# Optimization experiments

Hardware: AMD Instinct MI355X
Metric: run time of the kernel (lower is better)

Reference implementation:

```python
import jax, jax.numpy as jnp
import numpy as np

C = 64
D = C // 8  # query/key channels
B, H, W = 4, 64, 64


def setup_inputs() -> dict:
    key = jax.random.key(0)
    ks = jax.random.split(key, 8)
    x = jax.random.normal(ks[0], (B, C, H, W), dtype=jnp.float32)
    # 1x1 conv params (kernel squeezed to [out_ch, in_ch])
    sq = 1.0 / np.sqrt(C)
    Wq = jax.random.uniform(ks[1], (D, C), jnp.float32, -sq, sq)
    bq = jax.random.uniform(ks[2], (D,), jnp.float32, -sq, sq)
    Wk = jax.random.uniform(ks[3], (D, C), jnp.float32, -sq, sq)
    bk = jax.random.uniform(ks[4], (D,), jnp.float32, -sq, sq)
    Wv = jax.random.uniform(ks[5], (C, C), jnp.float32, -sq, sq)
    bv = jax.random.uniform(ks[6], (C,), jnp.float32, -sq, sq)
    # gamma is zero-initialized in the module; use a nonzero value so the
    # attention path actually contributes to the output.
    gamma = jax.random.normal(ks[7], (1,), dtype=jnp.float32)
    return {"x": x, "Wq": Wq, "bq": bq, "Wk": Wk, "bk": bk, "Wv": Wv, "bv": bv, "gamma": gamma}


def reference(x, Wq, bq, Wk, bk, Wv, bv, gamma):
    b, c, h, w = x.shape
    n = h * w
    xf = x.reshape(b, c, n)                                   # [B,C,N]
    q = jnp.einsum('dc,bcn->bdn', Wq, xf) + bq[None, :, None]  # [B,D,N]
    k = jnp.einsum('dc,bcn->bdn', Wk, xf) + bk[None, :, None]  # [B,D,N]
    v = jnp.einsum('ec,bcn->ben', Wv, xf) + bv[None, :, None]  # [B,C,N]
    energy = jnp.einsum('bdn,bdm->bnm', q, k)                  # [B,N,N] = Q^T K
    attn = jax.nn.softmax(energy, axis=-1)                     # softmax over keys m
    # out[b,c,n] = sum_m v[b,c,m] * attn[b,n,m]  (V @ attention^T in torch)
    out = jnp.einsum('bcm,bnm->bcn', v, attn).reshape(b, c, h, w)
    return gamma[0] * out + x
```

## Files before the change

### kernel.cpp

```cpp
#include <hip/hip_runtime.h>
#include <hip/hip_bf16.h>
#include <math.h>

#define BB 4
#define CC 64
#define DD 8
#define NN 4096
#define KS 8
#define KPS (NN / KS)
#define VSTR 260
#define KSTR 12
#define LOG2E 1.44269504088896340736f

typedef __attribute__((ext_vector_type(4))) short short4v;
typedef __attribute__((ext_vector_type(4))) unsigned short ushort4v;
typedef __attribute__((ext_vector_type(8))) unsigned short ushort8;
typedef __attribute__((ext_vector_type(16))) float f32x16;

#if defined(__HIP_DEVICE_COMPILE__)
  #if __has_builtin(__builtin_amdgcn_mfma_f32_32x32x8bf16_1k)
    #define MFMA32x8(A, B, C) __builtin_amdgcn_mfma_f32_32x32x8bf16_1k(A, B, C, 0, 0, 0)
  #elif __has_builtin(__builtin_amdgcn_mfma_f32_32x32x8_bf16)
    #define MFMA32x8(A, B, C) __builtin_amdgcn_mfma_f32_32x32x8_bf16(A, B, C, 0, 0, 0)
  #else
    #error "no 32x32x8 bf16 MFMA builtin in device pass"
  #endif
  #if __has_builtin(__builtin_amdgcn_exp2f)
    #define EXP2(x) __builtin_amdgcn_exp2f(x)
  #else
    #define EXP2(x) exp2f(x)
  #endif
#else
  static __device__ __host__ inline f32x16 MFMA32x8(short4v, short4v, f32x16 c) { return c; }
  #define EXP2(x) exp2f(x)
#endif

static __device__ inline short4v pack4(float a, float b, float c, float d) {
    union { short4v s; __hip_bfloat162 h[2]; } u;
    u.h[0] = __float22bfloat162_rn(make_float2(a, b));
    u.h[1] = __float22bfloat162_rn(make_float2(c, d));
    return u.s;
}
static __device__ inline unsigned packu(float lo, float hi) {
    union { __hip_bfloat162 h; unsigned u; } t;
    t.h = __float22bfloat162_rn(make_float2(lo, hi));
    return t.u;
}

__global__ __launch_bounds__(256) void qkv_kernel(
    const float* __restrict__ x,  const float* __restrict__ Wq, const float* __restrict__ bq,
    const float* __restrict__ Wk, const float* __restrict__ bk,
    const float* __restrict__ Wv, const float* __restrict__ bv,
    unsigned short* __restrict__ qb, unsigned short* __restrict__ kb,
    unsigned short* __restrict__ vT)
{
    __shared__ unsigned short LQ[128 * 8];
    __shared__ unsigned short LK[128 * 8];

    int tid = threadIdx.x;
    int wave = tid >> 6, lane = tid & 63;
    int l32 = lane & 31, h2 = lane >> 5;

    int blk = blockIdx.x;
    int b = blk & (BB - 1);
    int r2 = blk >> 2;
    int rt = r2 % 3;
    int ng = r2 / 3;
    int n0 = ng * 128 + wave * 32;

    short4v af[8];
    #pragma unroll
    for (int s = 0; s < 8; ++s) {
        float4 w4;
        if (rt < 2) {
            w4 = *(const float4*)(Wv + (size_t)(rt * 32 + l32) * CC + s * 8 + 4 * h2);
        } else if (l32 < 8) {
            w4 = *(const float4*)(Wq + (size_t)l32 * CC + s * 8 + 4 * h2);
        } else if (l32 < 16) {
            w4 = *(const float4*)(Wk + (size_t)(l32 - 8) * CC + s * 8 + 4 * h2);
        } else {
            w4 = make_float4(0.f, 0.f, 0.f, 0.f);
        }
        af[s] = pack4(w4.x, w4.y, w4.z, w4.w);
    }

    const float* xb = x + (size_t)b * CC * NN + n0 + l32;
    short4v bf[8];
    #pragma unroll
    for (int s = 0; s < 8; ++s) {
        int c0 = s * 8 + 4 * h2;
        float x0 = xb[(size_t)(c0 + 0) * NN];
        float x1 = xb[(size_t)(c0 + 1) * NN];
        float x2 = xb[(size_t)(c0 + 2) * NN];
        float x3 = xb[(size_t)(c0 + 3) * NN];
        bf[s] = pack4(x0, x1, x2, x3);
    }

    f32x16 acc;
    #pragma unroll
    for (int r = 0; r < 16; ++r) acc[r] = 0.f;
    #pragma unroll
    for (int s = 0; s < 8; ++s)
        acc = MFMA32x8(af[s], bf[s], acc);

    if (rt < 2) {
        #pragma unroll
        for (int r = 0; r < 16; ++r) {
            int row = rt * 32 + (r & 3) + 8 * (r >> 2) + 4 * h2;
            float val = acc[r] + bv[row];
            __hip_bfloat16 hv = __float2bfloat16(val);
            vT[((size_t)b * CC + row) * NN + n0 + l32] = *(unsigned short*)&hv;
        }
    } else {
        short4v qp = pack4((acc[0] + bq[0 + 4 * h2]) * LOG2E,
                           (acc[1] + bq[1 + 4 * h2]) * LOG2E,
                           (acc[2] + bq[2 + 4 * h2]) * LOG2E,
                           (acc[3] + bq[3 + 4 * h2]) * LOG2E);
        short4v kp = pack4(acc[4] + bk[0 + 4 * h2],
                           acc[5] + bk[1 + 4 * h2],
                           acc[6] + bk[2 + 4 * h2],
                           acc[7] + bk[3 + 4 * h2]);
        int nl = wave * 32 + l32;
        *(short4v*)(LQ + (size_t)nl * 8 + 4 * h2) = qp;
        *(short4v*)(LK + (size_t)nl * 8 + 4 * h2) = kp;
        __syncthreads();
        if (tid < 128) {
            ushort8 row = *(const ushort8*)(LQ + (size_t)tid * 8);
            *(ushort8*)(qb + ((size_t)b * NN + ng * 128 + tid) * 8) = row;
        } else {
            int t = tid - 128;
            ushort8 row = *(const ushort8*)(LK + (size_t)t * 8);
            *(ushort8*)(kb + ((size_t)b * NN + ng * 128 + t) * 8) = row;
        }
    }
}

__global__ __launch_bounds__(256, 4) void flash_kernel(
    const unsigned short* __restrict__ qb, const unsigned short* __restrict__ kb,
    const unsigned short* __restrict__ vT, unsigned* __restrict__ accb,
    float* __restrict__ sbuf)
{
    __shared__ unsigned short VS[64 * VSTR];
    __shared__ unsigned short KL[256 * KSTR];
    int tid = threadIdx.x;
    int wave = tid >> 6, lane = tid & 63;
    int l32 = lane & 31, h2 = lane >> 5;

    int blk = blockIdx.x;
    int b = blk & (BB - 1);
    int rest = blk >> 2;
    int split = rest & (KS - 1);
    int qchunk = rest >> 3;
    int n0 = qchunk * 128 + wave * 32;

    short4v qf = *(const short4v*)(qb + ((size_t)b * NN + n0 + l32) * DD + h2 * 4);

    const unsigned short* kbb = kb + (size_t)b * NN * DD;
    const unsigned short* vbb = vT + (size_t)b * CC * NN;
    int m0 = split * KPS;

    int chb = wave * 16 + h2;

    f32x16 o0, o1, zz;
    #pragma unroll
    for (int r = 0; r < 16; ++r) { o0[r] = 0.f; o1[r] = 0.f; zz[r] = 0.f; }
    float s0 = 0.f, s1 = 0.f, s2 = 0.f, s3 = 0.f;

    ushort8 vA[8];
    #pragma unroll
    for (int i = 0; i < 8; ++i)
        vA[i] = *(const ushort8*)(vbb + (size_t)(chb + 2 * i) * NN + m0 + l32 * 8);
    ushort8 kA = *(const ushort8*)(kbb + (size_t)(m0 + tid) * DD);
    #pragma unroll
    for (int i = 0; i < 8; ++i) {
        unsigned short* p = VS + (size_t)(chb + 2 * i) * VSTR + l32 * 8;
        *(ushort4v*)(p)     = *(ushort4v*)&vA[i];
        *(ushort4v*)(p + 4) = *((ushort4v*)&vA[i] + 1);
    }
    {
        unsigned short* p = KL + (size_t)tid * KSTR;
        *(ushort4v*)(p)     = *(ushort4v*)&kA;
        *(ushort4v*)(p + 4) = *((ushort4v*)&kA + 1);
    }
    __syncthreads();

    int mB = m0 + 256;
    ushort8 vB[8];
    #pragma unroll
    for (int i = 0; i < 8; ++i)
        vB[i] = *(const ushort8*)(vbb + (size_t)(chb + 2 * i) * NN + mB + l32 * 8);
    ushort8 kB = *(const ushort8*)(kbb + (size_t)(mB + tid) * DD);

    #pragma unroll
    for (int ph = 0; ph < 2; ++ph) {
        #pragma unroll
        for (int s = 0; s < 8; ++s) {
            short4v kf = *(const short4v*)(KL + (size_t)(s * 32 + l32) * KSTR + h2 * 4);
            f32x16 st = MFMA32x8(kf, qf, zz);
            float w[16];
            #pragma unroll
            for (int r = 0; r < 16; ++r) w[r] = EXP2(st[r]);
            s0 += (w[0] + w[1]) + (w[2] + w[3]);
            s1 += (w[4] + w[5]) + (w[6] + w[7]);
            s2 += (w[8] + w[9]) + (w[10] + w[11]);
            s3 += (w[12] + w[13]) + (w[14] + w[15]);

            union { short4v s; __hip_bfloat162 h[2]; } u[4];
            #pragma unroll
            for (int g = 0; g < 4; ++g) {
                u[g].h[0] = __float22bfloat162_rn(make_float2(w[4 * g],     w[4 * g + 1]));
                u[g].h[1] = __float22bfloat162_rn(make_float2(w[4 * g + 2], w[4 * g + 3]));
            }
            #pragma unroll
            for (int g = 0; g < 4; ++g) {
                int gg = s * 4 + g;
                short4v vf0 = *(const short4v*)(VS + (size_t)(l32)      * VSTR + gg * 8 + h2 * 4);
                short4v vf1 = *(const short4v*)(VS + (size_t)(32 + l32) * VSTR + gg * 8 + h2 * 4);
                o0 = MFMA32x8(u[g].s, vf0, o0);
                o1 = MFMA32x8(u[g].s, vf1, o1);
            }
        }
        if (ph == 0) {
            __syncthreads();
            #pragma unroll
            for (int i = 0; i < 8; ++i) {
                unsigned short* p = VS + (size_t)(chb + 2 * i) * VSTR + l32 * 8;
                *(ushort4v*)(p)     = *(ushort4v*)&vB[i];
                *(ushort4v*)(p + 4) = *((ushort4v*)&vB[i] + 1);
            }
            unsigned short* p = KL + (size_t)tid * KSTR;
            *(ushort4v*)(p)     = *(ushort4v*)&kB;
            *(ushort4v*)(p + 4) = *((ushort4v*)&kB + 1);
            __syncthreads();
        }
    }

    unsigned* au = accb + (((size_t)((b * KS + split) * 128 + qchunk * 4 + wave)) << 10);
    #pragma unroll
    for (int r = 0; r < 16; ++r)
        au[r * 64 + lane] = packu(o0[r], o1[r]);

    float ssum = (s0 + s1) + (s2 + s3);
    ssum += __shfl_xor(ssum, 32);
    if (lane < 32)
        sbuf[(size_t)(b * KS + split) * NN + n0 + l32] = ssum;
}

__global__ __launch_bounds__(256) void norm_kernel(
    const unsigned* __restrict__ accb, const float* __restrict__ sbuf,
    const float* __restrict__ x, const float* __restrict__ gamma,
    float* __restrict__ out)
{
    __shared__ float tile[32 * 65];
    __shared__ float stl[32];
    int blk = blockIdx.x;
    int b = blk >> 7;
    int g = blk & 127;
    int n0 = g * 32;
    int tid = threadIdx.x;

    if (tid < 32) {
        float st = 0.f;
        #pragma unroll
        for (int sp = 0; sp < KS; ++sp)
            st += sbuf[(size_t)(b * KS + sp) * NN + n0 + tid];
        stl[tid] = 1.0f / st;
    }

    int r = tid >> 4;
    int lane0 = (tid & 15) * 4;
    int h2 = lane0 >> 5;
    int qi = (r & 3) + 8 * (r >> 2) + 4 * h2;

    float alo[4], ahi[4];
    #pragma unroll
    for (int e = 0; e < 4; ++e) { alo[e] = 0.f; ahi[e] = 0.f; }
    #pragma unroll
    for (int sp = 0; sp < KS; ++sp) {
        const unsigned* base = accb + (((size_t)((b * KS + sp) * 128 + g)) << 10);
        uint4 v = *(const uint4*)(base + tid * 4);
        unsigned ws[4] = {v.x, v.y, v.z, v.w};
        #pragma unroll
        for (int e = 0; e < 4; ++e) {
            alo[e] += __uint_as_float(ws[e] << 16);
            ahi[e] += __uint_as_float(ws[e] & 0xFFFF0000u);
        }
    }
    #pragma unroll
    for (int e = 0; e < 4; ++e) {
        int cl = (lane0 + e) & 31;
        tile[qi * 65 + cl]      = alo[e];
        tile[qi * 65 + 32 + cl] = ahi[e];
    }
    __syncthreads();

    float gm = gamma[0];
    #pragma unroll
    for (int p = 0; p < 8; ++p) {
        int idx = p * 256 + tid;
        int c = idx >> 5, n_l = idx & 31;
        size_t xi = ((size_t)b * CC + c) * NN + n0 + n_l;
        out[xi] = gm * tile[n_l * 65 + c] * stl[n_l] + x[xi];
    }
}

extern "C" void kernel_launch(void* const* d_in, const int* in_sizes, int n_in,
                              void* d_out, int out_size, void* d_ws, size_t ws_size,
                              hipStream_t stream)
{
    const float* x     = (const float*)d_in[0];
    const float* Wq    = (const float*)d_in[1];
    const float* bq    = (const float*)d_in[2];
    const float* Wk    = (const float*)d_in[3];
    const float* bk    = (const float*)d_in[4];
    const float* Wv    = (const float*)d_in[5];
    const float* bv    = (const float*)d_in[6];
    const float* gamma = (const float*)d_in[7];
    float* out = (float*)d_out;

    float* ws = (float*)d_ws;
    size_t off = 0;
    unsigned short* qb = (unsigned short*)(ws + off); off += (size_t)BB * NN * DD / 2 + 64;
    unsigned short* kb = (unsigned short*)(ws + off); off += (size_t)BB * NN * DD / 2 + 64;
    unsigned short* vT = (unsigned short*)(ws + off); off += (size_t)BB * CC * NN / 2 + 64;
    unsigned* accb = (unsigned*)(ws + off); off += (size_t)BB * KS * NN * CC / 2;
    float* sbuf = ws + off; off += (size_t)BB * KS * NN;

    qkv_kernel<<<BB * 3 * 32, 256, 0, stream>>>(x, Wq, bq, Wk, bk, Wv, bv, qb, kb, vT);
    flash_kernel<<<BB * (NN / 128) * KS, 256, 0, stream>>>(qb, kb, vT, accb, sbuf);
    norm_kernel<<<BB * 128, 256, 0, stream>>>(accb, sbuf, x, gamma, out);
}
```

Measured before the change: 113.4 us.

## Use 512-thread flash blocks with 16 key splits and single-tile staging

Doubles the key-split count to 16 so each block processes one 256-key tile, and doubles the block to 512 threads (8 waves, 256 queries) so each staged K/V tile in LDS is reused by twice as many query rows. The two-phase double-buffered load is replaced by one cooperative load followed by the compute loop. This reduces K/V global reads per query and removes the mid-kernel barrier pair. In exchange it doubles the partial-accumulator and row-sum traffic the norm kernel must reduce, and it no longer overlaps loads with compute.

```diff
diff --git a/kernel.cpp b/kernel.cpp
--- a/kernel.cpp
+++ b/kernel.cpp
@@ -6,7 +6,7 @@
 #define CC 64
 #define DD 8
 #define NN 4096
-#define KS 8
+#define KS 16
 #define KPS (NN / KS)
 #define VSTR 260
 #define KSTR 12
@@ -135,7 +135,7 @@
     }
 }
 
-__global__ __launch_bounds__(256, 4) void flash_kernel(
+__global__ __launch_bounds__(512, 8) void flash_kernel(
     const unsigned short* __restrict__ qb, const unsigned short* __restrict__ kb,
     const unsigned short* __restrict__ vT, unsigned* __restrict__ accb,
     float* __restrict__ sbuf)
@@ -150,8 +150,8 @@
     int b = blk & (BB - 1);
     int rest = blk >> 2;
     int split = rest & (KS - 1);
-    int qchunk = rest >> 3;
-    int n0 = qchunk * 128 + wave * 32;
+    int qchunk = rest >> 4;
+    int n0 = qchunk * 256 + wave * 32;
 
     short4v qf = *(const short4v*)(qb + ((size_t)b * NN + n0 + l32) * DD + h2 * 4);
 
@@ -159,83 +159,67 @@
     const unsigned short* vbb = vT + (size_t)b * CC * NN;
     int m0 = split * KPS;
 
-    int chb = wave * 16 + h2;
+    int ch = tid >> 3, ks0 = (tid & 7) * 32;
+    {
+        const unsigned short* vg = vbb + (size_t)ch * NN + m0 + ks0;
+        ushort8 v0 = *(const ushort8*)(vg);
+        ushort8 v1 = *(const ushort8*)(vg + 8);
+        ushort8 v2 = *(const ushort8*)(vg + 16);
+        ushort8 v3 = *(const ushort8*)(vg + 24);
+        ushort8 kA = {0,0,0,0,0,0,0,0};
+        if (tid < 256) kA = *(const ushort8*)(kbb + (size_t)(m0 + tid) * DD);
+
+        unsigned short* vp = VS + (size_t)ch * VSTR + ks0;
+        *(ushort4v*)(vp)      = *(ushort4v*)&v0;
+        *(ushort4v*)(vp + 4)  = *((ushort4v*)&v0 + 1);
+        *(ushort4v*)(vp + 8)  = *(ushort4v*)&v1;
+        *(ushort4v*)(vp + 12) = *((ushort4v*)&v1 + 1);
+        *(ushort4v*)(vp + 16) = *(ushort4v*)&v2;
+        *(ushort4v*)(vp + 20) = *((ushort4v*)&v2 + 1);
+        *(ushort4v*)(vp + 24) = *(ushort4v*)&v3;
+        *(ushort4v*)(vp + 28) = *((ushort4v*)&v3 + 1);
+        if (tid < 256) {
+            unsigned short* p = KL + (size_t)tid * KSTR;
+            *(ushort4v*)(p)     = *(ushort4v*)&kA;
+            *(ushort4v*)(p + 4) = *((ushort4v*)&kA + 1);
+        }
+    }
+    __syncthreads();
 
     f32x16 o0, o1, zz;
     #pragma unroll
     for (int r = 0; r < 16; ++r) { o0[r] = 0.f; o1[r] = 0.f; zz[r] = 0.f; }
     float s0 = 0.f, s1 = 0.f, s2 = 0.f, s3 = 0.f;
 
-    ushort8 vA[8];
-    #pragma unroll
-    for (int i = 0; i < 8; ++i)
-        vA[i] = *(const ushort8*)(vbb + (size_t)(chb + 2 * i) * NN + m0 + l32 * 8);
-    ushort8 kA = *(const ushort8*)(kbb + (size_t)(m0 + tid) * DD);
-    #pragma unroll
-    for (int i = 0; i < 8; ++i) {
-        unsigned short* p = VS + (size_t)(chb + 2 * i) * VSTR + l32 * 8;
-        *(ushort4v*)(p)     = *(ushort4v*)&vA[i];
-        *(ushort4v*)(p + 4) = *((ushort4v*)&vA[i] + 1);
-    }
-    {
-        unsigned short* p = KL + (size_t)tid * KSTR;
-        *(ushort4v*)(p)     = *(ushort4v*)&kA;
-        *(ushort4v*)(p + 4) = *((ushort4v*)&kA + 1);
-    }
-    __syncthreads();
-
-    int mB = m0 + 256;
-    ushort8 vB[8];
-    #pragma unroll
-    for (int i = 0; i < 8; ++i)
-        vB[i] = *(const ushort8*)(vbb + (size_t)(chb + 2 * i) * NN + mB + l32 * 8);
-    ushort8 kB = *(const ushort8*)(kbb + (size_t)(mB + tid) * DD);
-
-    #pragma unroll
-    for (int ph = 0; ph < 2; ++ph) {
-        #pragma unroll
-        for (int s = 0; s < 8; ++s) {
-            short4v kf = *(const short4v*)(KL + (size_t)(s * 32 + l32) * KSTR + h2 * 4);
-            f32x16 st = MFMA32x8(kf, qf, zz);
-            float w[16];
-            #pragma unroll
-            for (int r = 0; r < 16; ++r) w[r] = EXP2(st[r]);
-            s0 += (w[0] + w[1]) + (w[2] + w[3]);
-            s1 += (w[4] + w[5]) + (w[6] + w[7]);
-            s2 += (w[8] + w[9]) + (w[10] + w[11]);
-            s3 += (w[12] + w[13]) + (w[14] + w[15]);
-
-            union { short4v s; __hip_bfloat162 h[2]; } u[4];
-            #pragma unroll
-            for (int g = 0; g < 4; ++g) {
-                u[g].h[0] = __float22bfloat162_rn(make_float2(w[4 * g],     w[4 * g + 1]));
-                u[g].h[1] = __float22bfloat162_rn(make_float2(w[4 * g + 2], w[4 * g + 3]));
-            }
-            #pragma unroll
-            for (int g = 0; g < 4; ++g) {
-                int gg = s * 4 + g;
-                short4v vf0 = *(const short4v*)(VS + (size_t)(l32)      * VSTR + gg * 8 + h2 * 4);
-                short4v vf1 = *(const short4v*)(VS + (size_t)(32 + l32) * VSTR + gg * 8 + h2 * 4);
-                o0 = MFMA32x8(u[g].s, vf0, o0);
-                o1 = MFMA32x8(u[g].s, vf1, o1);
-            }
-        }
-        if (ph == 0) {
-            __syncthreads();
-            #pragma unroll
-            for (int i = 0; i < 8; ++i) {
-                unsigned short* p = VS + (size_t)(chb + 2 * i) * VSTR + l32 * 8;
-                *(ushort4v*)(p)     = *(ushort4v*)&vB[i];
-                *(ushort4v*)(p + 4) = *((ushort4v*)&vB[i] + 1);
-            }
-            unsigned short* p = KL + (size_t)tid * KSTR;
-            *(ushort4v*)(p)     = *(ushort4v*)&kB;
-            *(ushort4v*)(p + 4) = *((ushort4v*)&kB + 1);
-            __syncthreads();
-        }
-    }
-
-    unsigned* au = accb + (((size_t)((b * KS + split) * 128 + qchunk * 4 + wave)) << 10);
+    #pragma unroll
+    for (int s = 0; s < 8; ++s) {
+        short4v kf = *(const short4v*)(KL + (size_t)(s * 32 + l32) * KSTR + h2 * 4);
+        f32x16 st = MFMA32x8(kf, qf, zz);
+        float w[16];
+        #pragma unroll
+        for (int r = 0; r < 16; ++r) w[r] = EXP2(st[r]);
+        s0 += (w[0] + w[1]) + (w[2] + w[3]);
+        s1 += (w[4] + w[5]) + (w[6] + w[7]);
+        s2 += (w[8] + w[9]) + (w[10] + w[11]);
+        s3 += (w[12] + w[13]) + (w[14] + w[15]);
+
+        union { short4v s; __hip_bfloat162 h[2]; } u[4];
+        #pragma unroll
+        for (int g = 0; g < 4; ++g) {
+            u[g].h[0] = __float22bfloat162_rn(make_float2(w[4 * g],     w[4 * g + 1]));
+            u[g].h[1] = __float22bfloat162_rn(make_float2(w[4 * g + 2], w[4 * g + 3]));
+        }
+        #pragma unroll
+        for (int g = 0; g < 4; ++g) {
+            int gg = s * 4 + g;
+            short4v vf0 = *(const short4v*)(VS + (size_t)(l32)      * VSTR + gg * 8 + h2 * 4);
+            short4v vf1 = *(const short4v*)(VS + (size_t)(32 + l32) * VSTR + gg * 8 + h2 * 4);
+            o0 = MFMA32x8(u[g].s, vf0, o0);
+            o1 = MFMA32x8(u[g].s, vf1, o1);
+        }
+    }
+
+    unsigned* au = accb + (((size_t)((b * KS + split) * 128 + qchunk * 8 + wave)) << 10);
     #pragma unroll
     for (int r = 0; r < 16; ++r)
         au[r * 64 + lane] = packu(o0[r], o1[r]);
@@ -327,6 +311,6 @@
     float* sbuf = ws + off; off += (size_t)BB * KS * NN;
 
     qkv_kernel<<<BB * 3 * 32, 256, 0, stream>>>(x, Wq, bq, Wk, bk, Wv, bv, qb, kb, vT);
-    flash_kernel<<<BB * (NN / 128) * KS, 256, 0, stream>>>(qb, kb, vT, accb, sbuf);
+    flash_kernel<<<BB * 16 * KS, 512, 0, stream>>>(qb, kb, vT, accb, sbuf);
     norm_kernel<<<BB * 128, 256, 0, stream>>>(accb, sbuf, x, gamma, out);
 }
```

Measured after the change: 105.2 us. 1.08x faster.
